# Optimization experiments

Measured on AMD Instinct MI355X. Metric: run time of the kernel, lower is better.

Reference implementation:

```python
import jax, jax.numpy as jnp
import numpy as np

E = 20    # number of residue types (rc.restypes)
NB = 2    # num_blocks per AngleHead
NA = 7    # num_angles
C_S = 384
C_H = 128
BS, L = 8, 2048


def setup_inputs() -> dict:
    key = jax.random.key(0)
    ks = jax.random.split(key, 16)
    sc = 0.02
    return {
        "s": jax.random.normal(ks[0], (BS, L, C_S), dtype=jnp.float32),
        "s_init": jax.random.normal(ks[1], (BS, L, C_S), dtype=jnp.float32),
        "aatype": jax.random.randint(ks[2], (BS, L), 0, E, dtype=jnp.int32),
        # stacked per-residue-type AngleHead params
        "Win": jax.random.normal(ks[3], (E, C_S, C_H), dtype=jnp.float32) * sc,
        "b_in": jax.random.normal(ks[4], (E, C_H), dtype=jnp.float32) * sc,
        "Winit": jax.random.normal(ks[5], (E, C_S, C_H), dtype=jnp.float32) * sc,
        "b_init2": jax.random.normal(ks[6], (E, C_H), dtype=jnp.float32) * sc,
        "Wb1": jax.random.normal(ks[7], (E, NB, C_H, C_H), dtype=jnp.float32) * sc,
        "bb1": jax.random.normal(ks[8], (E, NB, C_H), dtype=jnp.float32) * sc,
        "Wb2": jax.random.normal(ks[9], (E, NB, C_H, C_H), dtype=jnp.float32) * sc,
        "bb2": jax.random.normal(ks[10], (E, NB, C_H), dtype=jnp.float32) * sc,
        "Wout": jax.random.normal(ks[11], (E, C_H, NA * 2), dtype=jnp.float32) * sc,
        "b_out": jax.random.normal(ks[12], (E, NA * 2), dtype=jnp.float32) * sc,
    }


def reference(s, s_init, aatype, Win, b_in, Winit, b_init2, Wb1, bb1, Wb2, bb2, Wout, b_out):
    relu = jax.nn.relu
    bs, seq_len, c_s = s.shape
    N = bs * seq_len
    sf = s.reshape(N, c_s)          # [N, c_s]
    si = s_init.reshape(N, c_s)     # [N, c_s]

    # Dense dispatch: run every token through all E per-type heads, then
    # combine with the one-hot routing mask (math identical to the torch
    # gather/scatter loop over residue types).
    h = jnp.einsum('nd,edh->neh', relu(sf), Win) + b_in            # [N,E,H]
    h = h + jnp.einsum('nd,edh->neh', relu(si), Winit) + b_init2   # [N,E,H]

    for b in range(NB):  # ResidualBlock1d: s + W2 @ relu(W1 @ relu(s))
        a = jnp.einsum('neh,ehk->nek', relu(h), Wb1[:, b]) + bb1[:, b]
        a = jnp.einsum('nek,ekh->neh', relu(a), Wb2[:, b]) + bb2[:, b]
        h = h + a

    out = jnp.einsum('neh,eho->neo', relu(h), Wout) + b_out        # [N,E,2*NA]
    sel = jax.nn.one_hot(aatype.reshape(N), E, dtype=out.dtype)    # [N,E]
    ang = jnp.einsum('neo,ne->no', out, sel).reshape(bs, seq_len, NA, 2)

    # F.normalize(dim=-1): x / max(||x||, eps)
    nrm = jnp.maximum(jnp.linalg.norm(ang, axis=-1, keepdims=True), 1e-12)
    return ang / nrm
```

## Files before the change

### kernel.cpp

```cpp
#include <hip/hip_runtime.h>
#include <math.h>

#define E_TYPES 20
#define NBLK 2
#define NANG 7
#define CS 384
#define CH 128
#define N_TOK (8 * 2048)
#define TOK 32
#define TPB 256
#define TPB_MAIN 512
#define KC 128
#define MAX_TILES (N_TOK / TOK + E_TYPES)
#define NPREP 64

#define HIST_OFF 0

#define WT1_OFF (256 * 1024)
#define WT1_SZ  (20 * 8 * 24 * 2048)
#define WTR_OFF (WT1_OFF + WT1_SZ)

typedef __attribute__((ext_vector_type(8))) short bfrag;
typedef __attribute__((ext_vector_type(4))) float f32x4;
typedef unsigned short (*arr136)[136];

__device__ __forceinline__ void split_bf16(float x, unsigned short& h, unsigned short& l) {
    unsigned int u = __float_as_uint(x);
    unsigned int hb = (u + 0x7FFFu + ((u >> 16) & 1u)) & 0xFFFF0000u;
    h = (unsigned short)(hb >> 16);
    float r = x - __uint_as_float(hb);
    unsigned int v = __float_as_uint(r);
    l = (unsigned short)((v + 0x7FFFu + ((v >> 16) & 1u)) >> 16);
}

__global__ void prep1(const float* __restrict__ Win, const float* __restrict__ Winit,
                      const float* __restrict__ Wb1, const float* __restrict__ Wb2,
                      const int* __restrict__ aatype, int* __restrict__ wsI,
                      unsigned short* __restrict__ wt) {
    __shared__ int lh[E_TYPES];
    int bid = blockIdx.x;
    int t = threadIdx.x;
    if (bid >= 1600) {
        int b2 = bid - 1600;
        if (t < E_TYPES) lh[t] = 0;
        __syncthreads();
        int idx = b2 * 256 + t;
        if (idx < N_TOK) atomicAdd(&lh[aatype[idx]], 1);
        __syncthreads();
        if (t < E_TYPES) wsI[HIST_OFF + b2 * E_TYPES + t] = lh[t];
        return;
    }
    int gid = bid * 256 + t;
    unsigned short h[8], l[8];
    if (gid < 245760) {
        int lane = gid & 63;
        int bi = gid >> 6;
        int kb = bi % 24;
        int r = bi / 24;
        int nt = r & 7, e = r >> 3;
        int n = nt * 16 + (lane & 15);
        int k0 = kb * 32 + (lane >> 4) * 8;
        #pragma unroll
        for (int j = 0; j < 8; j++) {
            int k = k0 + j;
            float x = (k < CS) ? Win[((size_t)e * CS + k) * CH + n]
                               : Winit[((size_t)e * CS + (k - CS)) * CH + n];
            split_bf16(x, h[j], l[j]);
        }
        unsigned short* dst = wt + (WT1_OFF / 2) + (size_t)bi * 1024 + lane * 8;
        *(bfrag*)dst = *(bfrag*)h;
        *(bfrag*)(dst + 512) = *(bfrag*)l;
    } else {
        gid -= 245760;
        int lane = gid & 63;
        int bi = gid >> 6;
        int kb = bi & 3;
        int nt = (bi >> 2) & 7;
        int m4 = (bi >> 5) & 3;
        int e = bi >> 7;
        int b = m4 >> 1;
        const float* W = (m4 & 1) ? Wb2 : Wb1;
        int n = nt * 16 + (lane & 15);
        int k0 = kb * 32 + (lane >> 4) * 8;
        #pragma unroll
        for (int j = 0; j < 8; j++) {
            int k = k0 + j;
            float x = W[(((size_t)e * NBLK + b) * CH + k) * CH + n];
            split_bf16(x, h[j], l[j]);
        }
        unsigned short* dst = wt + (WTR_OFF / 2) + (size_t)bi * 1024 + lane * 8;
        *(bfrag*)dst = *(bfrag*)h;
        *(bfrag*)(dst + 512) = *(bfrag*)l;
    }
}

#define MFMA(a, b, c) __builtin_amdgcn_mfma_f32_16x16x32_bf16((a), (b), (c), 0, 0, 0)

__global__ __launch_bounds__(TPB_MAIN)
void angle_main(const float* __restrict__ s, const float* __restrict__ si,
                const float* __restrict__ b_in, const float* __restrict__ b_init2,
                const float* __restrict__ bb1, const float* __restrict__ bb2,
                const float* __restrict__ Wout, const float* __restrict__ b_out,
                const int* __restrict__ aatype,
                const int* __restrict__ wsI, const unsigned short* __restrict__ wt,
                float* __restrict__ out)
{
    #define BUFSZ 17408
    __shared__ __align__(16) char pool[2 * BUFSZ];
    __shared__ int ptok[TOK];
    __shared__ int cntS[E_TYPES];

    arr136 AH0 = (arr136)(pool);
    arr136 AL0 = (arr136)(pool + 8704);
    arr136 AH1 = (arr136)(pool + BUFSZ);
    arr136 AL1 = (arr136)(pool + BUFSZ + 8704);
    float (*Hf)[132] = (float (*)[132])(pool);
    float (*Of)[16]  = (float (*)[16])(pool + BUFSZ);

    int t = threadIdx.x;
    int w = t >> 6, lane = t & 63;
    int lane15 = lane & 15, quad = lane >> 4;

    int bid = blockIdx.x;
    const int q = MAX_TILES >> 3, r = MAX_TILES & 7;
    int xcd = bid & 7, sub = bid >> 3;
    int tile = (xcd < r ? xcd * (q + 1) : r * (q + 1) + (xcd - r) * q) + sub;

    if (w == 0 && lane < E_TYPES) {
        int c = 0;
        #pragma unroll
        for (int b = 0; b < NPREP; b++) c += wsI[HIST_OFF + b * E_TYPES + lane];
        cntS[lane] = c;
    }
    __syncthreads();

    int pos = tile * TOK;
    int e = -1, poff_e = 0;
    {
        int acc = 0;
        #pragma unroll
        for (int ee = 0; ee < E_TYPES; ee++) {
            int pad = (cntS[ee] + TOK - 1) & ~(TOK - 1);
            if (e < 0 && pos < acc + pad) { e = ee; poff_e = acc; }
            acc += pad;
        }
        if (pos >= acc) return;
    }
    int pos_in = pos - poff_e;
    int cnt_e = cntS[e];
    int n = cnt_e - pos_in; if (n > TOK) n = TOK;

    if (w == 0) {
        int hb = wsI[HIST_OFF + lane * E_TYPES + e];
        int inc = hb;
        #pragma unroll
        for (int d = 1; d < 64; d <<= 1) { int v = __shfl_up(inc, d); if (lane >= d) inc += v; }
        int pre = inc - hb;
        unsigned long long mle = __ballot(pre <= pos_in);
        int cb = 63 - __clzll(mle);
        int running = __shfl(pre, cb);
        int base = cb * 256;
        int lim = pos_in + n;
        while (running < lim && base < N_TOK) {
            const int4 a4 = *(const int4*)&aatype[base + lane * 4];
            int m0 = (a4.x == e), m1 = (a4.y == e), m2 = (a4.z == e), m3 = (a4.w == e);
            int c = m0 + m1 + m2 + m3;
            int incl = c;
            #pragma unroll
            for (int d = 1; d < 64; d <<= 1) { int v = __shfl_up(incl, d); if (lane >= d) incl += v; }
            int rk = running + incl - c;
            int tk = base + lane * 4;
            if (m0) { if (rk >= pos_in && rk < lim) ptok[rk - pos_in] = tk;     rk++; }
            if (m1) { if (rk >= pos_in && rk < lim) ptok[rk - pos_in] = tk + 1; rk++; }
            if (m2) { if (rk >= pos_in && rk < lim) ptok[rk - pos_in] = tk + 2; rk++; }
            if (m3) { if (rk >= pos_in && rk < lim) ptok[rk - pos_in] = tk + 3; rk++; }
            running += __shfl(incl, 63);
            base += 256;
        }
        int t0 = ptok[0];
        if (lane >= n && lane < TOK) ptok[lane] = t0;
    }
    __syncthreads();

    int nc = w * 16 + lane15;
    const bfrag* wt1 = (const bfrag*)((const char*)wt + WT1_OFF);
    const bfrag* wtr = (const bfrag*)((const char*)wt + WTR_OFF);

    f32x4 acc[2];
    {
        float bv = b_in[e * CH + nc] + b_init2[e * CH + nc];
        acc[0] = (f32x4){bv, bv, bv, bv};
        acc[1] = acc[0];
    }

    int srow = t >> 4;
    int scol = (t & 15) * 8;
    size_t rowoff = (size_t)ptok[srow] * CS + scol;
    float4 p0 = *(const float4*)(s + rowoff);
    float4 p1 = *(const float4*)(s + rowoff + 4);
    size_t wb = (size_t)(e * 8 + w) * 24;
    bfrag pbh = wt1[wb * 128 + lane];
    bfrag pbl = wt1[wb * 128 + 64 + lane];

    #pragma unroll
    for (int c = 0; c < 6; c++) {
        arr136 WAH = (c & 1) ? AH1 : AH0;
        arr136 WAL = (c & 1) ? AL1 : AL0;
        {
            float xv[8] = {p0.x, p0.y, p0.z, p0.w, p1.x, p1.y, p1.z, p1.w};
            unsigned short h8[8], l8[8];
            #pragma unroll
            for (int j = 0; j < 8; j++)
                split_bf16(fmaxf(xv[j], 0.f), h8[j], l8[j]);
            *(bfrag*)&WAH[srow][scol] = *(bfrag*)h8;
            *(bfrag*)&WAL[srow][scol] = *(bfrag*)l8;
        }
        if (c < 5) {
            const float* src = (c + 1 < 3) ? s : si;
            int kb0 = ((c + 1 < 3) ? (c + 1) : (c - 2)) * KC;
            p0 = *(const float4*)(src + rowoff + kb0);
            p1 = *(const float4*)(src + rowoff + kb0 + 4);
        }
        __syncthreads();
        #pragma unroll
        for (int ks = 0; ks < 4; ks++) {
            int kb = c * 4 + ks;
            bfrag bh = ks ? wt1[(wb + kb) * 128 + lane]      : pbh;
            bfrag bl = ks ? wt1[(wb + kb) * 128 + 64 + lane] : pbl;
            int kl = ks * 32 + quad * 8;
            bfrag ah0 = *(const bfrag*)&WAH[lane15][kl];
            bfrag ah1 = *(const bfrag*)&WAH[16 + lane15][kl];
            bfrag al0 = *(const bfrag*)&WAL[lane15][kl];
            bfrag al1 = *(const bfrag*)&WAL[16 + lane15][kl];
            acc[0] = MFMA(ah0, bh, acc[0]);
            acc[0] = MFMA(ah0, bl, acc[0]);
            acc[0] = MFMA(al0, bh, acc[0]);
            acc[1] = MFMA(ah1, bh, acc[1]);
            acc[1] = MFMA(ah1, bl, acc[1]);
            acc[1] = MFMA(al1, bh, acc[1]);
        }
        if (c < 5) {
            pbh = wt1[(wb + (c + 1) * 4) * 128 + lane];
            pbl = wt1[(wb + (c + 1) * 4) * 128 + 64 + lane];
        }
    }

    {
        size_t g0 = ((size_t)(e * 4) * 8 + w) * 4;
        pbh = wtr[g0 * 128 + lane];
        pbl = wtr[g0 * 128 + 64 + lane];
    }
    f32x4 cur[2] = {acc[0], acc[1]};
    #pragma unroll
    for (int g = 0; g < 4; g++) {
        arr136 WAH = (g & 1) ? AH1 : AH0;
        arr136 WAL = (g & 1) ? AL1 : AL0;
        #pragma unroll
        for (int mt = 0; mt < 2; mt++) {
            f32x4 v = cur[mt];
            #pragma unroll
            for (int rr = 0; rr < 4; rr++) {
                unsigned short hh, ll;
                split_bf16(fmaxf(v[rr], 0.f), hh, ll);
                WAH[mt * 16 + quad * 4 + rr][nc] = hh;
                WAL[mt * 16 + quad * 4 + rr][nc] = ll;
            }
        }
        __syncthreads();
        float bv = (g & 1) ? bb2[(e * NBLK + (g >> 1)) * CH + nc]
                           : bb1[(e * NBLK + (g >> 1)) * CH + nc];
        f32x4 r0 = (f32x4){bv, bv, bv, bv}, r1 = r0;
        size_t wgb = ((size_t)(e * 4 + g) * 8 + w) * 4;
        #pragma unroll
        for (int ks = 0; ks < 4; ks++) {
            bfrag bh = ks ? wtr[(wgb + ks) * 128 + lane]      : pbh;
            bfrag bl = ks ? wtr[(wgb + ks) * 128 + 64 + lane] : pbl;
            int kl = ks * 32 + quad * 8;
            bfrag ah0 = *(const bfrag*)&WAH[lane15][kl];
            bfrag ah1 = *(const bfrag*)&WAH[16 + lane15][kl];
            bfrag al0 = *(const bfrag*)&WAL[lane15][kl];
            bfrag al1 = *(const bfrag*)&WAL[16 + lane15][kl];
            r0 = MFMA(ah0, bh, r0);
            r0 = MFMA(ah0, bl, r0);
            r0 = MFMA(al0, bh, r0);
            r1 = MFMA(ah1, bh, r1);
            r1 = MFMA(ah1, bl, r1);
            r1 = MFMA(al1, bh, r1);
        }
        if (g < 3) {
            size_t nb = ((size_t)(e * 4 + g + 1) * 8 + w) * 4;
            pbh = wtr[nb * 128 + lane];
            pbl = wtr[nb * 128 + 64 + lane];
        }
        if (g & 1) { acc[0] += r0; acc[1] += r1; cur[0] = acc[0]; cur[1] = acc[1]; }
        else       { cur[0] = r0; cur[1] = r1; }
    }

    #pragma unroll
    for (int mt = 0; mt < 2; mt++) {
        f32x4 v = acc[mt];
        #pragma unroll
        for (int rr = 0; rr < 4; rr++)
            Hf[mt * 16 + quad * 4 + rr][nc] = fmaxf(v[rr], 0.f);
    }
    __syncthreads();

    const float* WoutE = Wout + (size_t)e * CH * (NANG * 2);
    const float* boutE = b_out + (size_t)e * (NANG * 2);
    for (int idx = t; idx < n * (NANG * 2); idx += TPB_MAIN) {
        int i = idx / (NANG * 2);
        int o = idx - i * (NANG * 2);
        float v0 = boutE[o], v1 = 0.f, v2 = 0.f, v3 = 0.f;
        #pragma unroll 4
        for (int k = 0; k < CH; k += 4) {
            v0 = fmaf(Hf[i][k],     WoutE[(size_t)k * (NANG * 2) + o],       v0);
            v1 = fmaf(Hf[i][k + 1], WoutE[(size_t)(k + 1) * (NANG * 2) + o], v1);
            v2 = fmaf(Hf[i][k + 2], WoutE[(size_t)(k + 2) * (NANG * 2) + o], v2);
            v3 = fmaf(Hf[i][k + 3], WoutE[(size_t)(k + 3) * (NANG * 2) + o], v3);
        }
        Of[i][o] = (v0 + v1) + (v2 + v3);
    }
    __syncthreads();

    for (int idx = t; idx < n * NANG; idx += TPB_MAIN) {
        int i = idx / NANG;
        int a = idx - i * NANG;
        float x = Of[i][2 * a];
        float y = Of[i][2 * a + 1];
        float nr = fmaxf(sqrtf(x * x + y * y), 1e-12f);
        size_t base = (size_t)ptok[i] * (NANG * 2) + 2 * a;
        out[base]     = x / nr;
        out[base + 1] = y / nr;
    }
}

extern "C" void kernel_launch(void* const* d_in, const int* in_sizes, int n_in,
                              void* d_out, int out_size, void* d_ws, size_t ws_size,
                              hipStream_t stream) {
    const float* s       = (const float*)d_in[0];
    const float* s_init  = (const float*)d_in[1];
    const int*   aatype  = (const int*)d_in[2];
    const float* Win     = (const float*)d_in[3];
    const float* b_in    = (const float*)d_in[4];
    const float* Winit   = (const float*)d_in[5];
    const float* b_init2 = (const float*)d_in[6];
    const float* Wb1     = (const float*)d_in[7];
    const float* bb1     = (const float*)d_in[8];
    const float* Wb2     = (const float*)d_in[9];
    const float* bb2     = (const float*)d_in[10];
    const float* Wout    = (const float*)d_in[11];
    const float* b_out   = (const float*)d_in[12];
    int* wsI = (int*)d_ws;
    unsigned short* wt = (unsigned short*)d_ws;
    float* out = (float*)d_out;

    hipLaunchKernelGGL(prep1, dim3(1664), dim3(256), 0, stream,
                       Win, Winit, Wb1, Wb2, aatype, wsI, wt);
    hipLaunchKernelGGL(angle_main, dim3(MAX_TILES), dim3(TPB_MAIN), 0, stream,
                       s, s_init, b_in, b_init2, bb1, bb2, Wout, b_out,
                       aatype, wsI, wt, out);
}
```

Before: 155.6 us.

## Software-pipeline weight and activation staging with split accumulators and lighter barriers

Restructures the main kernel's GEMM loops. Weight fragments are double-buffered and prefetched mid-iteration, and the next chunk's activation split and LDS store are issued after the current chunk's MFMAs. This lets one barrier per stage separate the double-buffered LDS tiles. Each MFMA chain is split into two independent accumulators to shorten the dependency chain. It also preloads biases early, swaps __syncthreads for a custom lgkmcnt wait plus s_barrier, and adds a min-blocks launch bound that may cap registers and cause spills.

New measurement: 161.0 us. 3.5% more time.

```diff
diff --git a/kernel.cpp b/kernel.cpp
--- a/kernel.cpp
+++ b/kernel.cpp
@@ -23,6 +23,12 @@
 typedef __attribute__((ext_vector_type(8))) short bfrag;
 typedef __attribute__((ext_vector_type(4))) float f32x4;
 typedef unsigned short (*arr136)[136];
+
+#define BAR() do { \
+    asm volatile("s_waitcnt lgkmcnt(0)" ::: "memory"); \
+    __builtin_amdgcn_s_barrier(); \
+    asm volatile("" ::: "memory"); \
+} while (0)
 
 __device__ __forceinline__ void split_bf16(float x, unsigned short& h, unsigned short& l) {
     unsigned int u = __float_as_uint(x);
@@ -96,7 +102,7 @@
 
 #define MFMA(a, b, c) __builtin_amdgcn_mfma_f32_16x16x32_bf16((a), (b), (c), 0, 0, 0)
 
-__global__ __launch_bounds__(TPB_MAIN)
+__global__ __launch_bounds__(TPB_MAIN, 4)
 void angle_main(const float* __restrict__ s, const float* __restrict__ si,
                 const float* __restrict__ b_in, const float* __restrict__ b_init2,
                 const float* __restrict__ bb1, const float* __restrict__ bb2,
@@ -132,23 +138,39 @@
         for (int b = 0; b < NPREP; b++) c += wsI[HIST_OFF + b * E_TYPES + lane];
         cntS[lane] = c;
     }
-    __syncthreads();
+    BAR();
 
     int pos = tile * TOK;
     int e = -1, poff_e = 0;
     {
-        int acc = 0;
+        int accT = 0;
         #pragma unroll
         for (int ee = 0; ee < E_TYPES; ee++) {
             int pad = (cntS[ee] + TOK - 1) & ~(TOK - 1);
-            if (e < 0 && pos < acc + pad) { e = ee; poff_e = acc; }
-            acc += pad;
-        }
-        if (pos >= acc) return;
+            if (e < 0 && pos < accT + pad) { e = ee; poff_e = accT; }
+            accT += pad;
+        }
+        if (pos >= accT) return;
     }
     int pos_in = pos - poff_e;
-    int cnt_e = cntS[e];
-    int n = cnt_e - pos_in; if (n > TOK) n = TOK;
+    int n = cntS[e] - pos_in; if (n > TOK) n = TOK;
+
+    int nc = w * 16 + lane15;
+    const bfrag* wt1 = (const bfrag*)((const char*)wt + WT1_OFF);
+    const bfrag* wtr = (const bfrag*)((const char*)wt + WTR_OFF);
+    size_t wb = (size_t)(e * 8 + w) * 24;
+
+    bfrag Bd[2][4];
+    {
+        const bfrag* nb = wt1 + wb * 128 + lane;
+        Bd[0][0] = nb[0];   Bd[0][1] = nb[128];
+        Bd[0][2] = nb[64];  Bd[0][3] = nb[192];
+    }
+    float bv_in  = b_in[e * CH + nc] + b_init2[e * CH + nc];
+    float bvb1a = bb1[(e * NBLK + 0) * CH + nc];
+    float bvb1b = bb1[(e * NBLK + 1) * CH + nc];
+    float bvb2a = bb2[(e * NBLK + 0) * CH + nc];
+    float bvb2b = bb2[(e * NBLK + 1) * CH + nc];
 
     if (w == 0) {
         int hb = wsI[HIST_OFF + lane * E_TYPES + e];
@@ -180,130 +202,159 @@
         int t0 = ptok[0];
         if (lane >= n && lane < TOK) ptok[lane] = t0;
     }
-    __syncthreads();
-
-    int nc = w * 16 + lane15;
-    const bfrag* wt1 = (const bfrag*)((const char*)wt + WT1_OFF);
-    const bfrag* wtr = (const bfrag*)((const char*)wt + WTR_OFF);
-
-    f32x4 acc[2];
-    {
-        float bv = b_in[e * CH + nc] + b_init2[e * CH + nc];
-        acc[0] = (f32x4){bv, bv, bv, bv};
-        acc[1] = acc[0];
-    }
+    BAR();
 
     int srow = t >> 4;
     int scol = (t & 15) * 8;
     size_t rowoff = (size_t)ptok[srow] * CS + scol;
     float4 p0 = *(const float4*)(s + rowoff);
     float4 p1 = *(const float4*)(s + rowoff + 4);
-    size_t wb = (size_t)(e * 8 + w) * 24;
-    bfrag pbh = wt1[wb * 128 + lane];
-    bfrag pbl = wt1[wb * 128 + 64 + lane];
+    {
+        float xv[8] = {p0.x, p0.y, p0.z, p0.w, p1.x, p1.y, p1.z, p1.w};
+        unsigned short h8[8], l8[8];
+        #pragma unroll
+        for (int j = 0; j < 8; j++) split_bf16(fmaxf(xv[j], 0.f), h8[j], l8[j]);
+        *(bfrag*)&AH0[srow][scol] = *(bfrag*)h8;
+        *(bfrag*)&AL0[srow][scol] = *(bfrag*)l8;
+    }
+    p0 = *(const float4*)(s + rowoff + KC);
+    p1 = *(const float4*)(s + rowoff + KC + 4);
+
+    f32x4 aA0 = (f32x4){bv_in, bv_in, bv_in, bv_in};
+    f32x4 aA1 = aA0;
+    f32x4 aB0 = (f32x4){0.f, 0.f, 0.f, 0.f};
+    f32x4 aB1 = aB0;
+    BAR();
 
     #pragma unroll
     for (int c = 0; c < 6; c++) {
         arr136 WAH = (c & 1) ? AH1 : AH0;
         arr136 WAL = (c & 1) ? AL1 : AL0;
-        {
-            float xv[8] = {p0.x, p0.y, p0.z, p0.w, p1.x, p1.y, p1.z, p1.w};
-            unsigned short h8[8], l8[8];
-            #pragma unroll
-            for (int j = 0; j < 8; j++)
-                split_bf16(fmaxf(xv[j], 0.f), h8[j], l8[j]);
-            *(bfrag*)&WAH[srow][scol] = *(bfrag*)h8;
-            *(bfrag*)&WAL[srow][scol] = *(bfrag*)l8;
-        }
-        if (c < 5) {
-            const float* src = (c + 1 < 3) ? s : si;
-            int kb0 = ((c + 1 < 3) ? (c + 1) : (c - 2)) * KC;
-            p0 = *(const float4*)(src + rowoff + kb0);
-            p1 = *(const float4*)(src + rowoff + kb0 + 4);
-        }
-        __syncthreads();
+        const bfrag* wbase = wt1 + (wb + c * 4) * 128 + lane;
+        bfrag c2h = wbase[256], c2l = wbase[320];
+        bfrag c3h = wbase[384], c3l = wbase[448];
         #pragma unroll
         for (int ks = 0; ks < 4; ks++) {
-            int kb = c * 4 + ks;
-            bfrag bh = ks ? wt1[(wb + kb) * 128 + lane]      : pbh;
-            bfrag bl = ks ? wt1[(wb + kb) * 128 + 64 + lane] : pbl;
+            bfrag bh = (ks == 0) ? Bd[c & 1][0] : (ks == 1) ? Bd[c & 1][1]
+                      : (ks == 2) ? c2h : c3h;
+            bfrag bl = (ks == 0) ? Bd[c & 1][2] : (ks == 1) ? Bd[c & 1][3]
+                      : (ks == 2) ? c2l : c3l;
             int kl = ks * 32 + quad * 8;
             bfrag ah0 = *(const bfrag*)&WAH[lane15][kl];
             bfrag ah1 = *(const bfrag*)&WAH[16 + lane15][kl];
             bfrag al0 = *(const bfrag*)&WAL[lane15][kl];
             bfrag al1 = *(const bfrag*)&WAL[16 + lane15][kl];
-            acc[0] = MFMA(ah0, bh, acc[0]);
-            acc[0] = MFMA(ah0, bl, acc[0]);
-            acc[0] = MFMA(al0, bh, acc[0]);
-            acc[1] = MFMA(ah1, bh, acc[1]);
-            acc[1] = MFMA(ah1, bl, acc[1]);
-            acc[1] = MFMA(al1, bh, acc[1]);
+            aA0 = MFMA(ah0, bh, aA0);
+            aB0 = MFMA(ah0, bl, aB0);
+            aB0 = MFMA(al0, bh, aB0);
+            aA1 = MFMA(ah1, bh, aA1);
+            aB1 = MFMA(ah1, bl, aB1);
+            aB1 = MFMA(al1, bh, aB1);
+            if (ks == 1) {
+                const bfrag* nb = (c < 5)
+                    ? wt1 + (wb + (c + 1) * 4) * 128 + lane
+                    : wtr + ((size_t)(e * 4 + 0) * 8 + w) * 4 * 128 + lane;
+                Bd[(c + 1) & 1][0] = nb[0];   Bd[(c + 1) & 1][1] = nb[128];
+                Bd[(c + 1) & 1][2] = nb[64];  Bd[(c + 1) & 1][3] = nb[192];
+            }
         }
         if (c < 5) {
-            pbh = wt1[(wb + (c + 1) * 4) * 128 + lane];
-            pbl = wt1[(wb + (c + 1) * 4) * 128 + 64 + lane];
-        }
-    }
-
+            arr136 NH = (c & 1) ? AH0 : AH1;
+            arr136 NL = (c & 1) ? AL0 : AL1;
+            float xv[8] = {p0.x, p0.y, p0.z, p0.w, p1.x, p1.y, p1.z, p1.w};
+            unsigned short h8[8], l8[8];
+            #pragma unroll
+            for (int j = 0; j < 8; j++) split_bf16(fmaxf(xv[j], 0.f), h8[j], l8[j]);
+            *(bfrag*)&NH[srow][scol] = *(bfrag*)h8;
+            *(bfrag*)&NL[srow][scol] = *(bfrag*)l8;
+            if (c < 4) {
+                const float* src = (c + 2 < 3) ? s : si;
+                int kb0 = ((c + 2 < 3) ? (c + 2) : (c - 1)) * KC;
+                p0 = *(const float4*)(src + rowoff + kb0);
+                p1 = *(const float4*)(src + rowoff + kb0 + 4);
+            }
+        }
+        BAR();
+    }
+
+    f32x4 h0 = aA0 + aB0;
+    f32x4 h1 = aA1 + aB1;
     {
-        size_t g0 = ((size_t)(e * 4) * 8 + w) * 4;
-        pbh = wtr[g0 * 128 + lane];
-        pbl = wtr[g0 * 128 + 64 + lane];
-    }
-    f32x4 cur[2] = {acc[0], acc[1]};
+        f32x4 cur[2] = {h0, h1};
+        #pragma unroll
+        for (int mt = 0; mt < 2; mt++) {
+            #pragma unroll
+            for (int rr = 0; rr < 4; rr++) {
+                unsigned short hh, ll;
+                split_bf16(fmaxf(cur[mt][rr], 0.f), hh, ll);
+                AH0[mt * 16 + quad * 4 + rr][nc] = hh;
+                AL0[mt * 16 + quad * 4 + rr][nc] = ll;
+            }
+        }
+    }
+    BAR();
+
     #pragma unroll
     for (int g = 0; g < 4; g++) {
         arr136 WAH = (g & 1) ? AH1 : AH0;
         arr136 WAL = (g & 1) ? AL1 : AL0;
-        #pragma unroll
-        for (int mt = 0; mt < 2; mt++) {
-            f32x4 v = cur[mt];
-            #pragma unroll
-            for (int rr = 0; rr < 4; rr++) {
-                unsigned short hh, ll;
-                split_bf16(fmaxf(v[rr], 0.f), hh, ll);
-                WAH[mt * 16 + quad * 4 + rr][nc] = hh;
-                WAL[mt * 16 + quad * 4 + rr][nc] = ll;
-            }
-        }
-        __syncthreads();
-        float bv = (g & 1) ? bb2[(e * NBLK + (g >> 1)) * CH + nc]
-                           : bb1[(e * NBLK + (g >> 1)) * CH + nc];
-        f32x4 r0 = (f32x4){bv, bv, bv, bv}, r1 = r0;
-        size_t wgb = ((size_t)(e * 4 + g) * 8 + w) * 4;
+        const bfrag* wbase = wtr + ((size_t)(e * 4 + g) * 8 + w) * 4 * 128 + lane;
+        bfrag c2h = wbase[256], c2l = wbase[320];
+        bfrag c3h = wbase[384], c3l = wbase[448];
+        float bv = (g & 1) ? ((g >> 1) ? bvb2b : bvb2a)
+                           : ((g >> 1) ? bvb1b : bvb1a);
+        f32x4 rA0 = (f32x4){bv, bv, bv, bv}, rA1 = rA0;
+        f32x4 rB0 = (f32x4){0.f, 0.f, 0.f, 0.f}, rB1 = rB0;
         #pragma unroll
         for (int ks = 0; ks < 4; ks++) {
-            bfrag bh = ks ? wtr[(wgb + ks) * 128 + lane]      : pbh;
-            bfrag bl = ks ? wtr[(wgb + ks) * 128 + 64 + lane] : pbl;
+            bfrag bh = (ks == 0) ? Bd[g & 1][0] : (ks == 1) ? Bd[g & 1][1]
+                      : (ks == 2) ? c2h : c3h;
+            bfrag bl = (ks == 0) ? Bd[g & 1][2] : (ks == 1) ? Bd[g & 1][3]
+                      : (ks == 2) ? c2l : c3l;
             int kl = ks * 32 + quad * 8;
             bfrag ah0 = *(const bfrag*)&WAH[lane15][kl];
             bfrag ah1 = *(const bfrag*)&WAH[16 + lane15][kl];
             bfrag al0 = *(const bfrag*)&WAL[lane15][kl];
             bfrag al1 = *(const bfrag*)&WAL[16 + lane15][kl];
-            r0 = MFMA(ah0, bh, r0);
-            r0 = MFMA(ah0, bl, r0);
-            r0 = MFMA(al0, bh, r0);
-            r1 = MFMA(ah1, bh, r1);
-            r1 = MFMA(ah1, bl, r1);
-            r1 = MFMA(al1, bh, r1);
-        }
+            rA0 = MFMA(ah0, bh, rA0);
+            rB0 = MFMA(ah0, bl, rB0);
+            rB0 = MFMA(al0, bh, rB0);
+            rA1 = MFMA(ah1, bh, rA1);
+            rB1 = MFMA(ah1, bl, rB1);
+            rB1 = MFMA(al1, bh, rB1);
+            if (ks == 1 && g < 3) {
+                const bfrag* nb = wtr + ((size_t)(e * 4 + g + 1) * 8 + w) * 4 * 128 + lane;
+                Bd[(g + 1) & 1][0] = nb[0];   Bd[(g + 1) & 1][1] = nb[128];
+                Bd[(g + 1) & 1][2] = nb[64];  Bd[(g + 1) & 1][3] = nb[192];
+            }
+        }
+        f32x4 r0 = rA0 + rB0, r1 = rA1 + rB1;
+        if (g & 1) { h0 += r0; h1 += r1; }
         if (g < 3) {
-            size_t nb = ((size_t)(e * 4 + g + 1) * 8 + w) * 4;
-            pbh = wtr[nb * 128 + lane];
-            pbl = wtr[nb * 128 + 64 + lane];
-        }
-        if (g & 1) { acc[0] += r0; acc[1] += r1; cur[0] = acc[0]; cur[1] = acc[1]; }
-        else       { cur[0] = r0; cur[1] = r1; }
-    }
-
-    #pragma unroll
-    for (int mt = 0; mt < 2; mt++) {
-        f32x4 v = acc[mt];
-        #pragma unroll
-        for (int rr = 0; rr < 4; rr++)
-            Hf[mt * 16 + quad * 4 + rr][nc] = fmaxf(v[rr], 0.f);
-    }
-    __syncthreads();
+            f32x4 cur0 = (g & 1) ? h0 : r0;
+            f32x4 cur1 = (g & 1) ? h1 : r1;
+            arr136 NH = (g & 1) ? AH0 : AH1;
+            arr136 NL = (g & 1) ? AL0 : AL1;
+            #pragma unroll
+            for (int rr = 0; rr < 4; rr++) {
+                unsigned short hh, ll;
+                split_bf16(fmaxf(cur0[rr], 0.f), hh, ll);
+                NH[quad * 4 + rr][nc] = hh;
+                NL[quad * 4 + rr][nc] = ll;
+                split_bf16(fmaxf(cur1[rr], 0.f), hh, ll);
+                NH[16 + quad * 4 + rr][nc] = hh;
+                NL[16 + quad * 4 + rr][nc] = ll;
+            }
+            BAR();
+        } else {
+            #pragma unroll
+            for (int rr = 0; rr < 4; rr++) {
+                Hf[quad * 4 + rr][nc]      = fmaxf(h0[rr], 0.f);
+                Hf[16 + quad * 4 + rr][nc] = fmaxf(h1[rr], 0.f);
+            }
+            BAR();
+        }
+    }
 
     const float* WoutE = Wout + (size_t)e * CH * (NANG * 2);
     const float* boutE = b_out + (size_t)e * (NANG * 2);
@@ -320,7 +371,7 @@
         }
         Of[i][o] = (v0 + v1) + (v2 + v3);
     }
-    __syncthreads();
+    BAR();
 
     for (int idx = t; idx < n * NANG; idx += TPB_MAIN) {
         int i = idx / NANG;
```
